# Kernel tuning notes

Hardware: AMD Instinct MI355X
Metric: run time of the kernel (lower is better)

Reference implementation:

```python
import jax, jax.numpy as jnp
import numpy as np

N = 100000   # nodes
E = 640000   # edges
F = 128      # num_features
D = 128      # dim
G = 128      # graphs in batch
BN_EPS = 1e-5


def setup_inputs() -> dict:
    key = jax.random.key(0)
    ks = jax.random.split(key, 16)
    lin = lambda k, i, o: (jax.random.normal(k, (i, o), jnp.float32) / np.sqrt(i)).astype(jnp.float32)
    inp = {
        "x": jax.random.normal(ks[0], (N, F), jnp.float32),
        "edge_index": jax.random.randint(ks[1], (2, E), 0, N),
        "batch": jnp.sort(jax.random.randint(ks[2], (N,), 0, G)),
        # layer 0: Linear(F,D)-ReLU-Linear(D,D), BN(D)
        "W0a": lin(ks[3], F, D), "b0a": jnp.zeros((D,), jnp.float32),
        "W0b": lin(ks[4], D, D), "b0b": jnp.zeros((D,), jnp.float32),
        "g0": jnp.ones((D,), jnp.float32), "be0": jnp.zeros((D,), jnp.float32),
        # layer 1: Linear(D,D)-ReLU-Linear(D,D), BN(D)
        "W1a": lin(ks[5], D, D), "b1a": jnp.zeros((D,), jnp.float32),
        "W1b": lin(ks[6], D, D), "b1b": jnp.zeros((D,), jnp.float32),
        "g1": jnp.ones((D,), jnp.float32), "be1": jnp.zeros((D,), jnp.float32),
        # layer 2: Linear(D,D)-ReLU-Linear(D,1), BN(1)
        "W2a": lin(ks[7], D, D), "b2a": jnp.zeros((D,), jnp.float32),
        "W2b": lin(ks[8], D, 1), "b2b": jnp.zeros((1,), jnp.float32),
        "g2": jnp.ones((1,), jnp.float32), "be2": jnp.zeros((1,), jnp.float32),
    }
    return inp


def _gin_layer(x, src, dst, Wa, ba, Wb, bb, g, be, relu_out):
    # GINConv (eps=0): h = x + sum_{j in N(i)} x_j, then MLP, then BN (train-mode stats)
    agg = jax.ops.segment_sum(x[src], dst, num_segments=N)
    h = x + agg
    h = jax.nn.relu(h @ Wa + ba) @ Wb + bb
    mu = jnp.mean(h, axis=0)
    var = jnp.mean((h - mu) ** 2, axis=0)  # biased var (torch BN normalization)
    h = (h - mu) * jax.lax.rsqrt(var + BN_EPS) * g + be
    return jax.nn.relu(h) if relu_out else h


def reference(x, edge_index, batch,
              W0a, b0a, W0b, b0b, g0, be0,
              W1a, b1a, W1b, b1b, g1, be1,
              W2a, b2a, W2b, b2b, g2, be2):
    src, dst = edge_index[0], edge_index[1]
    h = _gin_layer(x, src, dst, W0a, b0a, W0b, b0b, g0, be0, True)
    h = _gin_layer(h, src, dst, W1a, b1a, W1b, b1b, g1, be1, True)
    h = _gin_layer(h, src, dst, W2a, b2a, W2b, b2b, g2, be2, False)  # [N,1], no final ReLU
    # segment softmax over graphs, temperature 5.0 (PyG softmax semantics)
    z = h / 5.0
    m = jax.ops.segment_max(z, batch, num_segments=G)
    ez = jnp.exp(z - m[batch])
    s = jax.ops.segment_sum(ez, batch, num_segments=G)
    return ez / (s[batch] + 1e-16)
```

## Files before the change

kernel.cpp:

```cpp
#include <hip/hip_runtime.h>
#include <math.h>

#define NN 100000
#define EE 640000
#define GG 128
#define BN_EPS 1e-5f
#define NBLK 98

typedef __attribute__((ext_vector_type(8))) short short8;
typedef __attribute__((ext_vector_type(4))) float f32x4;


__device__ __forceinline__ short f2bf(float f) {
    unsigned u = __float_as_uint(f);
    u += 0x7fffu + ((u >> 16) & 1);
    return (short)(u >> 16);
}
__device__ __forceinline__ float bf2f(short s) {
    return __uint_as_float(((unsigned)(unsigned short)s) << 16);
}
__device__ __forceinline__ int swz(int row, int chunk) {
    return row * 128 + ((chunk ^ (row & 15)) << 3);
}
__device__ __forceinline__ int swze(int row, int col) {
    return row * 128 + (((col >> 3) ^ (row & 15)) << 3) + (col & 7);
}

__global__ void k_setup(const float* __restrict__ x,
                        const float* __restrict__ W0a, const float* __restrict__ W0b,
                        const float* __restrict__ W1a, const float* __restrict__ W1b,
                        const float* __restrict__ W2a, short* __restrict__ Wt,
                        short* __restrict__ Xbf, int* __restrict__ deg,
                        float* __restrict__ smf) {
    int idx = blockIdx.x * 256 + threadIdx.x;
    if (idx < 81920) {
        int wi = idx >> 14, r = idx & 16383;
        const float* W = (wi == 0) ? W0a : (wi == 1) ? W0b : (wi == 2) ? W1a
                        : (wi == 3) ? W1b : W2a;
        int k = r >> 7, n = r & 127;
        Wt[wi * 16384 + n * 128 + k] = f2bf(W[k * 128 + n]);
    }
    if (idx < NN) deg[idx] = 0;
    if (idx < 4112) smf[idx] = 0.0f;
    if (idx < 1600000) {
        const float4* xr = (const float4*)x + (size_t)idx * 2;
        float4 v0 = xr[0], v1 = xr[1];
        short8 o;
        o[0] = f2bf(v0.x); o[1] = f2bf(v0.y); o[2] = f2bf(v0.z); o[3] = f2bf(v0.w);
        o[4] = f2bf(v1.x); o[5] = f2bf(v1.y); o[6] = f2bf(v1.z); o[7] = f2bf(v1.w);
        *(short8*)(Xbf + (size_t)idx * 8) = o;
    }
}

__global__ void k_hist(const int* __restrict__ ei, int* __restrict__ deg) {
    int e = blockIdx.x * 256 + threadIdx.x;
    if (e < EE) atomicAdd(&deg[ei[EE + e]], 1);
}

__global__ __launch_bounds__(1024) void k_scan1(const int* __restrict__ deg,
                                                int* __restrict__ offs,
                                                int* __restrict__ bsums) {
    __shared__ int sm[1024];
    int t = threadIdx.x;
    int i = blockIdx.x * 1024 + t;
    int v = (i < NN) ? deg[i] : 0;
    sm[t] = v;
    __syncthreads();
    for (int off = 1; off < 1024; off <<= 1) {
        int add = (t >= off) ? sm[t - off] : 0;
        __syncthreads();
        sm[t] += add;
        __syncthreads();
    }
    if (i < NN) offs[i] = sm[t] - v;
    if (t == 1023) bsums[blockIdx.x] = sm[1023];
}

__global__ __launch_bounds__(1024) void k_scan3(int* __restrict__ offs,
                                                const int* __restrict__ bsums,
                                                int* __restrict__ pos) {
    __shared__ int smb[128];
    __shared__ int baseS;
    int t = threadIdx.x;
    if (t < 128) smb[t] = (t < NBLK) ? bsums[t] : 0;
    __syncthreads();
    if (t == 0) {
        int b = 0;
        for (int i = 0; i < (int)blockIdx.x; ++i) b += smb[i];
        baseS = b;
    }
    __syncthreads();
    int i = blockIdx.x * 1024 + t;
    if (i < NN) {
        int o = offs[i] + baseS;
        offs[i] = o;
        pos[i] = o;
    }
    if (i == 0) offs[NN] = EE;
}

__global__ void k_fill(const int* __restrict__ ei, int* __restrict__ pos,
                       int* __restrict__ csr) {
    int e = blockIdx.x * 256 + threadIdx.x;
    if (e < EE) {
        int d = ei[EE + e];
        int p = atomicAdd(&pos[d], 1);
        csr[p] = ei[e];
    }
}

template <int MODE>
__global__ __launch_bounds__(512, 4) void k_gmlp(const short* __restrict__ hin,
                                                 const int* __restrict__ offs,
                                                 const int* __restrict__ csr,
                                                 const float* __restrict__ rep,
                                                 const float* __restrict__ g,
                                                 const float* __restrict__ be,
                                                 const short* __restrict__ Wta,
                                                 const float* __restrict__ ba,
                                                 const short* __restrict__ Wtb,
                                                 const float* __restrict__ bb,
                                                 short* __restrict__ hout,
                                                 float* __restrict__ statsRep,
                                                 const float* __restrict__ w2,
                                                 const float* __restrict__ b2,
                                                 float* __restrict__ z,
                                                 float* __restrict__ s2rep) {
    __shared__ short Asb[16384];
    __shared__ short Wsb[16384];
    __shared__ float parS[128], parH[128];
    __shared__ float redS[1024];
    const int t = threadIdx.x;
    const int row0 = blockIdx.x * 128;
    const int lane = t & 63, wave = t >> 6;
    const int r16 = lane & 15, q = lane >> 4;
    const int rh = wave & 3, ch = wave >> 2;
    const int RA = rh * 32, CB = ch * 64;
    const int l = t & 15;

    if constexpr (MODE != 0) {
        if (t < 128) {
            float s = 0.f, ss = 0.f;
#pragma unroll
            for (int r = 0; r < 8; ++r) {
                s += rep[r * 256 + t];
                ss += rep[r * 256 + 128 + t];
            }
            const float inv = 1.0f / (float)NN;
            float mu = s * inv;
            float var = ss * inv - mu * mu;
            float sc = g[t] / sqrtf(var + BN_EPS);
            parS[t] = sc;
            parH[t] = be[t] - mu * sc;
        }
        __syncthreads();
    }

    short8 wpre[4];
#pragma unroll
    for (int i = 0; i < 4; ++i) {
        int f = i * 512 + t;
        int r = f >> 4, c8 = f & 15;
        *(short8*)&Wsb[swz(r, c8)] = *(const short8*)(Wta + r * 128 + c8 * 8);
        if constexpr (MODE != 2) wpre[i] = *(const short8*)(Wtb + r * 128 + c8 * 8);
    }

    float sc8[8], sh8[8];
    if constexpr (MODE != 0) {
#pragma unroll
        for (int j = 0; j < 8; ++j) { sc8[j] = parS[l * 8 + j]; sh8[j] = parH[l * 8 + j]; }
    }
#pragma unroll
    for (int p = 0; p < 4; ++p) {
        int r = p * 32 + (t >> 4);
        int gr = row0 + r;
        float f8[8] = {0.f, 0.f, 0.f, 0.f, 0.f, 0.f, 0.f, 0.f};
        if (gr < NN) {
            int j0 = offs[gr], j1 = offs[gr + 1];
            short8 v = *(const short8*)(hin + (size_t)gr * 128 + l * 8);
#pragma unroll
            for (int k = 0; k < 8; ++k)
                f8[k] = (MODE != 0) ? fmaxf(fmaf(bf2f(v[k]), sc8[k], sh8[k]), 0.f) : bf2f(v[k]);
            int j = j0;
            for (; j + 3 < j1; j += 4) {
                int s0 = csr[j], s1 = csr[j + 1], s2 = csr[j + 2], s3 = csr[j + 3];
                short8 w0 = *(const short8*)(hin + (size_t)s0 * 128 + l * 8);
                short8 w1 = *(const short8*)(hin + (size_t)s1 * 128 + l * 8);
                short8 w2v = *(const short8*)(hin + (size_t)s2 * 128 + l * 8);
                short8 w3 = *(const short8*)(hin + (size_t)s3 * 128 + l * 8);
#pragma unroll
                for (int k = 0; k < 8; ++k) {
                    if constexpr (MODE != 0) {
                        f8[k] += fmaxf(fmaf(bf2f(w0[k]), sc8[k], sh8[k]), 0.f)
                               + fmaxf(fmaf(bf2f(w1[k]), sc8[k], sh8[k]), 0.f)
                               + fmaxf(fmaf(bf2f(w2v[k]), sc8[k], sh8[k]), 0.f)
                               + fmaxf(fmaf(bf2f(w3[k]), sc8[k], sh8[k]), 0.f);
                    } else {
                        f8[k] += bf2f(w0[k]) + bf2f(w1[k]) + bf2f(w2v[k]) + bf2f(w3[k]);
                    }
                }
            }
            for (; j < j1; ++j) {
                int s0 = csr[j];
                short8 w0 = *(const short8*)(hin + (size_t)s0 * 128 + l * 8);
#pragma unroll
                for (int k = 0; k < 8; ++k)
                    f8[k] += (MODE != 0) ? fmaxf(fmaf(bf2f(w0[k]), sc8[k], sh8[k]), 0.f)
                                         : bf2f(w0[k]);
            }
        }
        short8 o;
#pragma unroll
        for (int k = 0; k < 8; ++k) o[k] = f2bf(f8[k]);
        *(short8*)&Asb[swz(r, l)] = o;
    }
    __syncthreads();

    f32x4 acc[2][4];
#pragma unroll
    for (int rt = 0; rt < 2; ++rt)
#pragma unroll
        for (int ct = 0; ct < 4; ++ct) acc[rt][ct] = (f32x4)0.f;
#pragma unroll
    for (int kk = 0; kk < 4; ++kk) {
        short8 b[4], a[2];
#pragma unroll
        for (int ct = 0; ct < 4; ++ct)
            b[ct] = *(const short8*)&Wsb[swz(CB + ct * 16 + r16, kk * 4 + q)];
#pragma unroll
        for (int rt = 0; rt < 2; ++rt)
            a[rt] = *(const short8*)&Asb[swz(RA + rt * 16 + r16, kk * 4 + q)];
#pragma unroll
        for (int rt = 0; rt < 2; ++rt)
#pragma unroll
            for (int ct = 0; ct < 4; ++ct)
                acc[rt][ct] = __builtin_amdgcn_mfma_f32_16x16x32_bf16(a[rt], b[ct], acc[rt][ct], 0, 0, 0);
    }
    __syncthreads();

    float bav[4];
#pragma unroll
    for (int ct = 0; ct < 4; ++ct) bav[ct] = ba[CB + ct * 16 + r16];
#pragma unroll
    for (int rt = 0; rt < 2; ++rt)
#pragma unroll
        for (int ct = 0; ct < 4; ++ct)
#pragma unroll
            for (int rg = 0; rg < 4; ++rg) {
                float m = fmaxf(acc[rt][ct][rg] + bav[ct], 0.f);
                Asb[swze(RA + rt * 16 + q * 4 + rg, CB + ct * 16 + r16)] = f2bf(m);
            }
    if constexpr (MODE != 2) {
#pragma unroll
        for (int i = 0; i < 4; ++i) {
            int f = i * 512 + t;
            int r = f >> 4, c8 = f & 15;
            *(short8*)&Wsb[swz(r, c8)] = wpre[i];
        }
    }
    __syncthreads();

    if constexpr (MODE == 2) {
        const int rr = t >> 4;
        float4 w0 = ((const float4*)w2)[l * 2];
        float4 w1 = ((const float4*)w2)[l * 2 + 1];
        float b2v = b2[0];
        float s = 0.f, ss = 0.f;
#pragma unroll
        for (int p = 0; p < 4; ++p) {
            int r = p * 32 + rr;
            int gr = row0 + r;
            short8 v = *(const short8*)&Asb[swz(r, l)];
            float pp = bf2f(v[0]) * w0.x + bf2f(v[1]) * w0.y + bf2f(v[2]) * w0.z +
                       bf2f(v[3]) * w0.w + bf2f(v[4]) * w1.x + bf2f(v[5]) * w1.y +
                       bf2f(v[6]) * w1.z + bf2f(v[7]) * w1.w;
#pragma unroll
            for (int off = 1; off < 16; off <<= 1) pp += __shfl_xor(pp, off, 16);
            if (l == 0 && gr < NN) {
                float h2 = pp + b2v;
                z[gr] = h2;
                s += h2;
                ss += h2 * h2;
            }
        }
        s += __shfl_xor(s, 16); s += __shfl_xor(s, 32);
        ss += __shfl_xor(ss, 16); ss += __shfl_xor(ss, 32);
        if ((t & 63) == 0) { redS[wave * 2] = s; redS[wave * 2 + 1] = ss; }
        __syncthreads();
        if (t == 0) {
            float S = 0.f, SS = 0.f;
#pragma unroll
            for (int w = 0; w < 8; ++w) { S += redS[w * 2]; SS += redS[w * 2 + 1]; }
            int rp = (blockIdx.x & 7) * 2;
            unsafeAtomicAdd(&s2rep[rp], S);
            unsafeAtomicAdd(&s2rep[rp + 1], SS);
        }
        return;
    } else {
#pragma unroll
        for (int rt = 0; rt < 2; ++rt)
#pragma unroll
            for (int ct = 0; ct < 4; ++ct) acc[rt][ct] = (f32x4)0.f;
#pragma unroll
        for (int kk = 0; kk < 4; ++kk) {
            short8 b[4], a[2];
#pragma unroll
            for (int ct = 0; ct < 4; ++ct)
                b[ct] = *(const short8*)&Wsb[swz(CB + ct * 16 + r16, kk * 4 + q)];
#pragma unroll
            for (int rt = 0; rt < 2; ++rt)
                a[rt] = *(const short8*)&Asb[swz(RA + rt * 16 + r16, kk * 4 + q)];
#pragma unroll
            for (int rt = 0; rt < 2; ++rt)
#pragma unroll
                for (int ct = 0; ct < 4; ++ct)
                    acc[rt][ct] = __builtin_amdgcn_mfma_f32_16x16x32_bf16(a[rt], b[ct], acc[rt][ct], 0, 0, 0);
        }
        __syncthreads();

        float bbv[4];
#pragma unroll
        for (int ct = 0; ct < 4; ++ct) bbv[ct] = bb[CB + ct * 16 + r16];
        float s[4] = {0.f, 0.f, 0.f, 0.f}, ss[4] = {0.f, 0.f, 0.f, 0.f};
#pragma unroll
        for (int rt = 0; rt < 2; ++rt)
#pragma unroll
            for (int ct = 0; ct < 4; ++ct)
#pragma unroll
                for (int rg = 0; rg < 4; ++rg) {
                    int lr = RA + rt * 16 + q * 4 + rg;
                    int gr = row0 + lr;
                    float hv = acc[rt][ct][rg] + bbv[ct];
                    if (gr < NN) { s[ct] += hv; ss[ct] += hv * hv; }
                    Asb[swze(lr, CB + ct * 16 + r16)] = f2bf(hv);
                }
#pragma unroll
        for (int ct = 0; ct < 4; ++ct) {
            s[ct] += __shfl_xor(s[ct], 16);
            s[ct] += __shfl_xor(s[ct], 32);
            ss[ct] += __shfl_xor(ss[ct], 16);
            ss[ct] += __shfl_xor(ss[ct], 32);
        }
        if (lane < 16) {
#pragma unroll
            for (int ct = 0; ct < 4; ++ct) {
                int col = CB + ct * 16 + r16;
                redS[rh * 256 + col] = s[ct];
                redS[rh * 256 + 128 + col] = ss[ct];
            }
        }
        __syncthreads();
        if (t < 256) {
            float v = redS[t] + redS[256 + t] + redS[512 + t] + redS[768 + t];
            unsafeAtomicAdd(&statsRep[(blockIdx.x & 7) * 256 + t], v);
        }
#pragma unroll
        for (int i = 0; i < 4; ++i) {
            int f = i * 512 + t;
            int r = f >> 4, c8 = f & 15;
            int gr = row0 + r;
            if (gr < NN)
                *(short8*)(hout + (size_t)gr * 128 + c8 * 8) = *(const short8*)&Asb[swz(r, c8)];
        }
    }
}

__device__ __forceinline__ int lbound(const int* __restrict__ b, int val) {
    int lo = 0, hi = NN;
    while (lo < hi) {
        int m = (lo + hi) >> 1;
        if (b[m] < val) lo = m + 1; else hi = m;
    }
    return lo;
}

__global__ void k_softmax(const float* __restrict__ zr, const float* __restrict__ s2rep,
                          const float* __restrict__ g2, const float* __restrict__ be2,
                          const int* __restrict__ batch, float* __restrict__ out) {
    __shared__ float rb[4];
    const int g = blockIdx.x, t = threadIdx.x;
    const int lo = lbound(batch, g), hi = lbound(batch, g + 1);
    float s = 0.f, ssq = 0.f;
#pragma unroll
    for (int i = 0; i < 8; ++i) { s += s2rep[i * 2]; ssq += s2rep[i * 2 + 1]; }
    const float mu = s / (float)NN;
    const float var = ssq / (float)NN - mu * mu;
    const float sc = g2[0] / sqrtf(var + BN_EPS) * 0.2f;
    const float sh = (be2[0] - mu * g2[0] / sqrtf(var + BN_EPS)) * 0.2f;

    float m = -INFINITY;
    for (int i = lo + t; i < hi; i += 256) m = fmaxf(m, fmaf(zr[i], sc, sh));
#pragma unroll
    for (int off = 1; off < 64; off <<= 1) m = fmaxf(m, __shfl_xor(m, off, 64));
    if ((t & 63) == 0) rb[t >> 6] = m;
    __syncthreads();
    float gmax = fmaxf(fmaxf(rb[0], rb[1]), fmaxf(rb[2], rb[3]));
    __syncthreads();

    float sum = 0.f;
    for (int i = lo + t; i < hi; i += 256) {
        float e = expf(fmaf(zr[i], sc, sh) - gmax);
        out[i] = e;
        sum += e;
    }
#pragma unroll
    for (int off = 1; off < 64; off <<= 1) sum += __shfl_xor(sum, off, 64);
    if ((t & 63) == 0) rb[t >> 6] = sum;
    __syncthreads();
    float S = rb[0] + rb[1] + rb[2] + rb[3];
    float inv = 1.0f / (S + 1e-16f);
    for (int i = lo + t; i < hi; i += 256) out[i] *= inv;
}

extern "C" void kernel_launch(void* const* d_in, const int* in_sizes, int n_in,
                              void* d_out, int out_size, void* d_ws, size_t ws_size,
                              hipStream_t stream) {
    const float* x   = (const float*)d_in[0];
    const int* ei    = (const int*)d_in[1];
    const int* batch = (const int*)d_in[2];
    const float *W0a = (const float*)d_in[3],  *b0a = (const float*)d_in[4];
    const float *W0b = (const float*)d_in[5],  *b0b = (const float*)d_in[6];
    const float *g0  = (const float*)d_in[7],  *be0 = (const float*)d_in[8];
    const float *W1a = (const float*)d_in[9],  *b1a = (const float*)d_in[10];
    const float *W1b = (const float*)d_in[11], *b1b = (const float*)d_in[12];
    const float *g1  = (const float*)d_in[13], *be1 = (const float*)d_in[14];
    const float *W2a = (const float*)d_in[15], *b2a = (const float*)d_in[16];
    const float *W2b = (const float*)d_in[17], *b2b = (const float*)d_in[18];
    const float *g2  = (const float*)d_in[19], *be2 = (const float*)d_in[20];
    float* out = (float*)d_out;

    char* wsb = (char*)d_ws;
    short* Abf = (short*)wsb;
    short* Bbf = (short*)(wsb + 25600000);
    float* Zb  = (float*)(wsb + 51200000);
    float* SMf = (float*)(wsb + 51600000);
    float* S0r = SMf;
    float* S1r = SMf + 2048;
    float* S2r = SMf + 4096;
    int* offs  = (int*)(wsb + 51620000);
    int* bsums = (int*)(wsb + 52020004);
    int* csr   = (int*)(wsb + 52020516);
    short* Wt  = (short*)(wsb + 54580544);
    short* Xbf = (short*)(wsb + 54744384);
    int* deg = (int*)wsb;
    int* pos = (int*)(wsb + 400000);

    const int gE    = (EE + 255) / 256;
    const int gGmlp = (NN + 127) / 128;

    k_setup<<<6250, 256, 0, stream>>>(x, W0a, W0b, W1a, W1b, W2a, Wt, Xbf, deg, SMf);

    k_hist<<<gE, 256, 0, stream>>>(ei, deg);
    k_scan1<<<NBLK, 1024, 0, stream>>>(deg, offs, bsums);
    k_scan3<<<NBLK, 1024, 0, stream>>>(offs, bsums, pos);
    k_fill<<<gE, 256, 0, stream>>>(ei, pos, csr);

    k_gmlp<0><<<gGmlp, 512, 0, stream>>>(Xbf, offs, csr, nullptr, nullptr, nullptr,
                                         Wt, b0a, Wt + 16384, b0b, Abf, S0r,
                                         nullptr, nullptr, nullptr, nullptr);
    k_gmlp<1><<<gGmlp, 512, 0, stream>>>(Abf, offs, csr, S0r, g0, be0,
                                         Wt + 2 * 16384, b1a, Wt + 3 * 16384, b1b, Bbf, S1r,
                                         nullptr, nullptr, nullptr, nullptr);
    k_gmlp<2><<<gGmlp, 512, 0, stream>>>(Bbf, offs, csr, S1r, g1, be1,
                                         Wt + 4 * 16384, b2a, nullptr, nullptr,
                                         nullptr, nullptr, W2b, b2b, Zb, S2r);

    k_softmax<<<GG, 256, 0, stream>>>(Zb, S2r, g2, be2, batch, out);
}
```

Baseline: 372.7 us.

## Pre-pack weights in MFMA fragment order, read from global, drop weight LDS

Weights are pre-permuted in k_setup into per-lane MFMA B-fragment order, so each wave loads its B operands straight from global/L2 instead of staging them through a 32KB shared buffer. This halves LDS per block and launch bounds go from 4 to 8 blocks per CU to raise occupancy for the latency-bound gather phase. The neighbor-gather loop is also restructured into a single 4-wide masked loop with clamped indices, removing the scalar tail loop at the cost of redundant loads and FMAs for the padded entries. The risk is extra global/L2 traffic for repeated weight reads and register pressure under the tighter launch bound.

```diff
diff --git a/kernel.cpp b/kernel.cpp
--- a/kernel.cpp
+++ b/kernel.cpp
@@ -38,7 +38,11 @@
         const float* W = (wi == 0) ? W0a : (wi == 1) ? W0b : (wi == 2) ? W1a
                         : (wi == 3) ? W1b : W2a;
         int k = r >> 7, n = r & 127;
-        Wt[wi * 16384 + n * 128 + k] = f2bf(W[k * 128 + n]);
+        int ch = n >> 6, ct = (n >> 4) & 3, r16 = n & 15;
+        int kc = k >> 3, kk = kc >> 2, q = kc & 3, e = k & 7;
+        int lane = r16 + (q << 4);
+        Wt[wi * 16384 + ((((ch * 4 + ct) * 4 + kk) * 64 + lane) << 3) + e] =
+            f2bf(W[k * 128 + n]);
     }
     if (idx < NN) deg[idx] = 0;
     if (idx < 4112) smf[idx] = 0.0f;
@@ -110,7 +114,7 @@
 }
 
 template <int MODE>
-__global__ __launch_bounds__(512, 4) void k_gmlp(const short* __restrict__ hin,
+__global__ __launch_bounds__(512, 8) void k_gmlp(const short* __restrict__ hin,
                                                  const int* __restrict__ offs,
                                                  const int* __restrict__ csr,
                                                  const float* __restrict__ rep,
@@ -127,7 +131,6 @@
                                                  float* __restrict__ z,
                                                  float* __restrict__ s2rep) {
     __shared__ short Asb[16384];
-    __shared__ short Wsb[16384];
     __shared__ float parS[128], parH[128];
     __shared__ float redS[1024];
     const int t = threadIdx.x;
@@ -156,14 +159,8 @@
         __syncthreads();
     }
 
-    short8 wpre[4];
-#pragma unroll
-    for (int i = 0; i < 4; ++i) {
-        int f = i * 512 + t;
-        int r = f >> 4, c8 = f & 15;
-        *(short8*)&Wsb[swz(r, c8)] = *(const short8*)(Wta + r * 128 + c8 * 8);
-        if constexpr (MODE != 2) wpre[i] = *(const short8*)(Wtb + r * 128 + c8 * 8);
-    }
+    const short* wA = Wta + (size_t)((ch * 1024 + lane) << 3);
+    const short* wB = (MODE != 2) ? (Wtb + (size_t)((ch * 1024 + lane) << 3)) : nullptr;
 
     float sc8[8], sh8[8];
     if constexpr (MODE != 0) {
@@ -181,9 +178,13 @@
 #pragma unroll
             for (int k = 0; k < 8; ++k)
                 f8[k] = (MODE != 0) ? fmaxf(fmaf(bf2f(v[k]), sc8[k], sh8[k]), 0.f) : bf2f(v[k]);
-            int j = j0;
-            for (; j + 3 < j1; j += 4) {
-                int s0 = csr[j], s1 = csr[j + 1], s2 = csr[j + 2], s3 = csr[j + 3];
+            int jlast = j1 - 1;
+            for (int j = j0; j < j1; j += 4) {
+                float m1 = (j + 1 <= jlast) ? 1.f : 0.f;
+                float m2 = (j + 2 <= jlast) ? 1.f : 0.f;
+                float m3 = (j + 3 <= jlast) ? 1.f : 0.f;
+                int i1 = min(j + 1, jlast), i2 = min(j + 2, jlast), i3 = min(j + 3, jlast);
+                int s0 = csr[j], s1 = csr[i1], s2 = csr[i2], s3 = csr[i3];
                 short8 w0 = *(const short8*)(hin + (size_t)s0 * 128 + l * 8);
                 short8 w1 = *(const short8*)(hin + (size_t)s1 * 128 + l * 8);
                 short8 w2v = *(const short8*)(hin + (size_t)s2 * 128 + l * 8);
@@ -191,23 +192,18 @@
 #pragma unroll
                 for (int k = 0; k < 8; ++k) {
                     if constexpr (MODE != 0) {
-                        f8[k] += fmaxf(fmaf(bf2f(w0[k]), sc8[k], sh8[k]), 0.f)
-                               + fmaxf(fmaf(bf2f(w1[k]), sc8[k], sh8[k]), 0.f)
-                               + fmaxf(fmaf(bf2f(w2v[k]), sc8[k], sh8[k]), 0.f)
-                               + fmaxf(fmaf(bf2f(w3[k]), sc8[k], sh8[k]), 0.f);
+                        f8[k] += fmaxf(fmaf(bf2f(w0[k]), sc8[k], sh8[k]), 0.f);
+                        f8[k] = fmaf(m1, fmaxf(fmaf(bf2f(w1[k]), sc8[k], sh8[k]), 0.f), f8[k]);
+                        f8[k] = fmaf(m2, fmaxf(fmaf(bf2f(w2v[k]), sc8[k], sh8[k]), 0.f), f8[k]);
+                        f8[k] = fmaf(m3, fmaxf(fmaf(bf2f(w3[k]), sc8[k], sh8[k]), 0.f), f8[k]);
                     } else {
-                        f8[k] += bf2f(w0[k]) + bf2f(w1[k]) + bf2f(w2v[k]) + bf2f(w3[k]);
+                        f8[k] += bf2f(w0[k]);
+                        f8[k] = fmaf(m1, bf2f(w1[k]), f8[k]);
+                        f8[k] = fmaf(m2, bf2f(w2v[k]), f8[k]);
+                        f8[k] = fmaf(m3, bf2f(w3[k]), f8[k]);
                     }
                 }
             }
-            for (; j < j1; ++j) {
-                int s0 = csr[j];
-                short8 w0 = *(const short8*)(hin + (size_t)s0 * 128 + l * 8);
-#pragma unroll
-                for (int k = 0; k < 8; ++k)
-                    f8[k] += (MODE != 0) ? fmaxf(fmaf(bf2f(w0[k]), sc8[k], sh8[k]), 0.f)
-                                         : bf2f(w0[k]);
-            }
         }
         short8 o;
 #pragma unroll
@@ -226,7 +222,7 @@
         short8 b[4], a[2];
 #pragma unroll
         for (int ct = 0; ct < 4; ++ct)
-            b[ct] = *(const short8*)&Wsb[swz(CB + ct * 16 + r16, kk * 4 + q)];
+            b[ct] = *(const short8*)(wA + ((ct * 4 + kk) << 9));
 #pragma unroll
         for (int rt = 0; rt < 2; ++rt)
             a[rt] = *(const short8*)&Asb[swz(RA + rt * 16 + r16, kk * 4 + q)];
@@ -250,14 +246,6 @@
                 float m = fmaxf(acc[rt][ct][rg] + bav[ct], 0.f);
                 Asb[swze(RA + rt * 16 + q * 4 + rg, CB + ct * 16 + r16)] = f2bf(m);
             }
-    if constexpr (MODE != 2) {
-#pragma unroll
-        for (int i = 0; i < 4; ++i) {
-            int f = i * 512 + t;
-            int r = f >> 4, c8 = f & 15;
-            *(short8*)&Wsb[swz(r, c8)] = wpre[i];
-        }
-    }
     __syncthreads();
 
     if constexpr (MODE == 2) {
@@ -306,7 +294,7 @@
             short8 b[4], a[2];
 #pragma unroll
             for (int ct = 0; ct < 4; ++ct)
-                b[ct] = *(const short8*)&Wsb[swz(CB + ct * 16 + r16, kk * 4 + q)];
+                b[ct] = *(const short8*)(wB + ((ct * 4 + kk) << 9));
 #pragma unroll
             for (int rt = 0; rt < 2; ++rt)
                 a[rt] = *(const short8*)&Asb[swz(RA + rt * 16 + r16, kk * 4 + q)];
```

Result: slower. 517.4 us (+38.8%).
